# Performance work log

Measured on AMD Instinct MI355X. Metric: run time of the kernel, lower is better.

Reference implementation:

```python
import jax, jax.numpy as jnp
import numpy as np
import math

B, N, D, S = 128, 2048, 512, 64  # batch, nodes, d_model, state_features


def setup_inputs() -> dict:
    key = jax.random.key(0)
    k1, k2, k3, k4, k5 = jax.random.split(key, 5)
    node_embeddings = jax.random.normal(k1, (B, N, D), dtype=jnp.float32)
    truck_state = jax.random.normal(k2, (B, S), dtype=jnp.float32)
    mask = jax.random.bernoulli(k3, 0.3, (B, N))  # True = masked-out node
    Wq = jax.random.normal(k4, (D, S), dtype=jnp.float32) * 0.05  # query_proj weight
    bq = jnp.zeros((D,), dtype=jnp.float32)
    Ws = jax.random.normal(k5, (D, D), dtype=jnp.float32) * 0.02  # scores_proj weight
    bs = jnp.zeros((D,), dtype=jnp.float32)
    return {"node_embeddings": node_embeddings, "truck_state": truck_state,
            "mask": mask, "Wq": Wq, "bq": bq, "Ws": Ws, "bs": bs}


def reference(node_embeddings, truck_state, mask, Wq, bq, Ws, bs):
    d_model = node_embeddings.shape[-1]
    scale = 1.0 / math.sqrt(d_model)
    # query = query_proj(truck_state): [B, D]
    query = truck_state @ Wq.T + bq
    # single-query attention scores over nodes: [B, N]
    attn_scores = jnp.einsum('bd,bnd->bn', query, node_embeddings) * scale
    attn_scores = jnp.where(mask, -jnp.inf, attn_scores)
    attn_weights = jax.nn.softmax(attn_scores, axis=-1)
    # context: [B, D]
    context = jnp.einsum('bn,bnd->bd', attn_weights, node_embeddings)
    # scores = scores_proj(context): [B, D]
    scores = context @ Ws.T + bs
    # dot-product logits per node: [B, N]
    logits = jnp.einsum('bnd,bd->bn', node_embeddings, scores) * scale
    logits = jnp.where(mask, -jnp.inf, logits)
    return logits
```

## Files before the change

kernel.cpp:

```cpp
#include <hip/hip_runtime.h>
#include <math.h>

#define BB 128
#define NN 2048
#define DD 512
#define SS 64
#define NCH 16
#define CH (NN / NCH)
#define NPW (CH / 8)
#define SCALE 0.044194173824159216f
#define NEG_BIG (-1.0e30f)

__device__ __forceinline__ float dot8(float4 a0, float4 a1, float4 b0, float4 b1) {
    return a0.x*b0.x + a0.y*b0.y + a0.z*b0.z + a0.w*b0.w
         + a1.x*b1.x + a1.y*b1.y + a1.z*b1.z + a1.w*b1.w;
}

__global__ __launch_bounds__(512, 8) void k_pass1(
    const float* __restrict__ node, const unsigned char* __restrict__ mask,
    const float* __restrict__ ts, const float* __restrict__ Wq,
    const float* __restrict__ bq,
    float* __restrict__ part_ctx, float* __restrict__ part_l)
{
    int bid   = blockIdx.x;
    int b     = bid >> 4;
    int chunk = bid & 15;
    int wave  = threadIdx.x >> 6;
    int lane  = threadIdx.x & 63;
    int dbase = lane * 8;

    __shared__ float q_lds[DD];
    __shared__ float lds_ctx[8][DD];
    __shared__ float lds_l[8];

    {
        int d = threadIdx.x;
        const float4* tv = (const float4*)(ts + b * SS);
        const float4* wv = (const float4*)(Wq + (size_t)d * SS);
        float acc = 0.f;
#pragma unroll
        for (int k = 0; k < SS / 4; ++k) {
            float4 a = tv[k], w = wv[k];
            acc += a.x*w.x + a.y*w.y + a.z*w.z + a.w*w.w;
        }
        q_lds[d] = acc + bq[d];
    }

    int n0 = chunk * CH + wave * NPW;
    const unsigned char* mrow = mask + (size_t)b * NN;
    unsigned long long bal = __ballot(mrow[n0 + (lane & 15)] == 0);
    unsigned int lv = (unsigned int)(bal & 0xffffull);
    __syncthreads();

    float4 q0 = *(const float4*)&q_lds[dbase];
    float4 q1 = *(const float4*)&q_lds[dbase + 4];

    float l = 0.f;
    float c0=0,c1=0,c2=0,c3=0,c4=0,c5=0,c6=0,c7=0;
    const float* basep = node + ((size_t)b * NN + n0) * DD + dbase;

    while (lv) {
        int j0 = __ffs(lv) - 1; lv &= lv - 1;
        bool has2 = (lv != 0);
        int j1 = has2 ? (__ffs(lv) - 1) : j0;
        lv = has2 ? (lv & (lv - 1)) : lv;
        const float* r0 = basep + (size_t)j0 * DD;
        const float* r1 = basep + (size_t)j1 * DD;
        float4 v0a = *(const float4*)r0, v0b = *(const float4*)(r0 + 4);
        float4 v1a = *(const float4*)r1, v1b = *(const float4*)(r1 + 4);
        float dp0 = dot8(q0, q1, v0a, v0b);
        float dp1 = dot8(q0, q1, v1a, v1b);
#pragma unroll
        for (int off = 32; off; off >>= 1) {
            dp0 += __shfl_xor(dp0, off, 64);
            dp1 += __shfl_xor(dp1, off, 64);
        }
        float p0 = __expf(dp0 * SCALE);
        float p1 = has2 ? __expf(dp1 * SCALE) : 0.f;
        l += p0 + p1;
        c0 += p0*v0a.x + p1*v1a.x;
        c1 += p0*v0a.y + p1*v1a.y;
        c2 += p0*v0a.z + p1*v1a.z;
        c3 += p0*v0a.w + p1*v1a.w;
        c4 += p0*v0b.x + p1*v1b.x;
        c5 += p0*v0b.y + p1*v1b.y;
        c6 += p0*v0b.z + p1*v1b.z;
        c7 += p0*v0b.w + p1*v1b.w;
    }

    if (lane == 0) lds_l[wave] = l;
    *(float4*)&lds_ctx[wave][dbase]     = make_float4(c0, c1, c2, c3);
    *(float4*)&lds_ctx[wave][dbase + 4] = make_float4(c4, c5, c6, c7);
    __syncthreads();
    {
        int d = threadIdx.x;
        float acc = 0.f;
#pragma unroll
        for (int w = 0; w < 8; ++w) acc += lds_ctx[w][d];
        part_ctx[(size_t)bid * DD + d] = acc;
    }
    if (threadIdx.x == 0) {
        float L = 0.f;
#pragma unroll
        for (int w = 0; w < 8; ++w) L += lds_l[w];
        part_l[bid] = L;
    }
}

__global__ __launch_bounds__(256) void k_scores(
    const float* __restrict__ part_ctx, const float* __restrict__ part_l,
    const float* __restrict__ Ws, const float* __restrict__ bs,
    float* __restrict__ scores)
{
    int b    = blockIdx.x >> 2;
    int qt   = blockIdx.x & 3;
    int wave = threadIdx.x >> 6;
    int lane = threadIdx.x & 63;
    int dbase = lane * 8;
    __shared__ float ctx[DD];

    float L = 0.f;
#pragma unroll
    for (int c = 0; c < NCH; ++c) L += part_l[(b << 4) | c];
    float Linv = 1.f / fmaxf(L, 1e-30f);

    for (int d = threadIdx.x; d < DD; d += 256) {
        float acc = 0.f;
#pragma unroll
        for (int c = 0; c < NCH; ++c)
            acc += part_ctx[(size_t)((b << 4) | c) * DD + d];
        ctx[d] = acc * Linv;
    }
    __syncthreads();

    float4 x0 = *(const float4*)&ctx[dbase];
    float4 x1 = *(const float4*)&ctx[dbase + 4];
    for (int j = 0; j < 32; ++j) {
        int dd = qt * 128 + wave * 32 + j;
        const float* wrow = Ws + (size_t)dd * DD + dbase;
        float4 w0 = *(const float4*)wrow;
        float4 w1 = *(const float4*)(wrow + 4);
        float dp = dot8(x0, x1, w0, w1);
#pragma unroll
        for (int off = 32; off; off >>= 1) dp += __shfl_xor(dp, off, 64);
        if (lane == 0) scores[b * DD + dd] = dp + bs[dd];
    }
}

__global__ __launch_bounds__(256, 8) void k_logits(
    const float* __restrict__ node, const unsigned char* __restrict__ mask,
    const float* __restrict__ scores, float* __restrict__ out)
{
    int wave = threadIdx.x >> 6;
    int lane = threadIdx.x & 63;
    int dbase = lane * 8;
    int wg = blockIdx.x * 4 + wave;
    int rg = 32767 - wg;
    int g0 = rg * 8;
    int b  = g0 >> 11;

    unsigned long long mb = *(const unsigned long long*)(mask + g0);

    if (lane < 8 && ((mb >> (8 * lane)) & 0xffull)) out[g0 + lane] = NEG_BIG;

    unsigned int lv = 0;
#pragma unroll
    for (int i = 0; i < 8; ++i)
        lv |= (((mb >> (8 * i)) & 0xffull) == 0ull ? 1u : 0u) << i;

    const float* sc = scores + b * DD + dbase;
    float4 t0 = *(const float4*)sc;
    float4 t1 = *(const float4*)(sc + 4);
    const float* basep = node + (size_t)g0 * DD + dbase;

    while (lv) {
        int j0 = __ffs(lv) - 1; lv &= lv - 1;
        bool has2 = (lv != 0);
        int j1 = has2 ? (__ffs(lv) - 1) : j0;
        lv = has2 ? (lv & (lv - 1)) : lv;
        const float* r0 = basep + (size_t)j0 * DD;
        const float* r1 = basep + (size_t)j1 * DD;
        float4 v0a = *(const float4*)r0, v0b = *(const float4*)(r0 + 4);
        float4 v1a = *(const float4*)r1, v1b = *(const float4*)(r1 + 4);
        float dp0 = dot8(t0, t1, v0a, v0b);
        float dp1 = dot8(t0, t1, v1a, v1b);
#pragma unroll
        for (int off = 32; off; off >>= 1) {
            dp0 += __shfl_xor(dp0, off, 64);
            dp1 += __shfl_xor(dp1, off, 64);
        }
        if (lane == 0) {
            out[g0 + j0] = dp0 * SCALE;
            if (has2) out[g0 + j1] = dp1 * SCALE;
        }
    }
}

extern "C" void kernel_launch(void* const* d_in, const int* in_sizes, int n_in,
                              void* d_out, int out_size, void* d_ws, size_t ws_size,
                              hipStream_t stream)
{
    const float*         node = (const float*)d_in[0];
    const float*         ts   = (const float*)d_in[1];
    const unsigned char* mask = (const unsigned char*)d_in[2];
    const float*         Wq   = (const float*)d_in[3];
    const float*         bq   = (const float*)d_in[4];
    const float*         Ws   = (const float*)d_in[5];
    const float*         bs   = (const float*)d_in[6];
    float* out = (float*)d_out;

    float* ws       = (float*)d_ws;
    float* part_ctx = ws;
    float* part_l   = part_ctx + BB * NCH * DD;
    float* scores   = part_l + BB * NCH;

    k_pass1 <<<BB * NCH, 512, 0, stream>>>(node, mask, ts, Wq, bq,
                                           part_ctx, part_l);
    k_scores<<<BB * 4, 256, 0, stream>>>(part_ctx, part_l, Ws, bs, scores);
    k_logits<<<(BB * NN) / 32, 256, 0, stream>>>(node, mask, scores, out);
}
```

Before: 202.3 us.

## Balance unmasked rows across waves via block-level compacted node lists

Both node-streaming kernels now build a compacted list of unmasked node indices per block in shared memory using ballots and prefix popcounts. The rows are dealt round-robin across the waves, so each wave handles an even share instead of a fixed contiguous slice whose unmasked count varies. The intent is to cut wave-level load imbalance, where a block waits on its slowest wave. The cost is an extra barrier, shared-memory traffic for the list, and shuffles to fetch the row indices.

```diff
diff --git a/kernel.cpp b/kernel.cpp
--- a/kernel.cpp
+++ b/kernel.cpp
@@ -7,7 +7,6 @@
 #define SS 64
 #define NCH 16
 #define CH (NN / NCH)
-#define NPW (CH / 8)
 #define SCALE 0.044194173824159216f
 #define NEG_BIG (-1.0e30f)
 
@@ -28,10 +27,13 @@
     int wave  = threadIdx.x >> 6;
     int lane  = threadIdx.x & 63;
     int dbase = lane * 8;
+    int n0    = chunk * CH;
 
     __shared__ float q_lds[DD];
     __shared__ float lds_ctx[8][DD];
     __shared__ float lds_l[8];
+    __shared__ unsigned long long bal_lds[2];
+    __shared__ unsigned char list_lds[CH];
 
     {
         int d = threadIdx.x;
@@ -46,26 +48,47 @@
         q_lds[d] = acc + bq[d];
     }
 
-    int n0 = chunk * CH + wave * NPW;
-    const unsigned char* mrow = mask + (size_t)b * NN;
-    unsigned long long bal = __ballot(mrow[n0 + (lane & 15)] == 0);
-    unsigned int lv = (unsigned int)(bal & 0xffffull);
+    int t = threadIdx.x;
+    if (t < CH) {
+        bool ok = (mask[(size_t)b * NN + n0 + t] == 0);
+        unsigned long long balw = __ballot(ok);
+        if ((t & 63) == 0) bal_lds[t >> 6] = balw;
+    }
+    __syncthreads();
+    unsigned long long b0 = bal_lds[0], b1 = bal_lds[1];
+    int cnt0 = __popcll(b0);
+    int K    = cnt0 + __popcll(b1);
+    if (t < CH) {
+        bool ok = ((t < 64 ? b0 : b1) >> (t & 63)) & 1ull;
+        if (ok) {
+            int rank = (t < 64)
+                ? __popcll(b0 & ((1ull << t) - 1ull))
+                : cnt0 + __popcll(b1 & ((1ull << (t - 64)) - 1ull));
+            list_lds[rank] = (unsigned char)t;
+        }
+    }
     __syncthreads();
 
     float4 q0 = *(const float4*)&q_lds[dbase];
     float4 q1 = *(const float4*)&q_lds[dbase + 4];
+
+    int nmine = (K > wave) ? (K - wave + 7) >> 3 : 0;
+    int src = wave + 8 * (lane < 16 ? lane : 15);
+    if (src >= K) src = (K > 0) ? K - 1 : 0;
+    int myidx = list_lds[src];
 
     float l = 0.f;
     float c0=0,c1=0,c2=0,c3=0,c4=0,c5=0,c6=0,c7=0;
     const float* basep = node + ((size_t)b * NN + n0) * DD + dbase;
 
-    while (lv) {
-        int j0 = __ffs(lv) - 1; lv &= lv - 1;
-        bool has2 = (lv != 0);
-        int j1 = has2 ? (__ffs(lv) - 1) : j0;
-        lv = has2 ? (lv & (lv - 1)) : lv;
-        const float* r0 = basep + (size_t)j0 * DD;
-        const float* r1 = basep + (size_t)j1 * DD;
+    int npairs = (nmine + 1) >> 1;
+    for (int jp = 0; jp < npairs; ++jp) {
+        int j0 = 2 * jp, j1 = 2 * jp + 1;
+        bool has2 = (j1 < nmine);
+        int i0 = __shfl(myidx, j0);
+        int i1 = __shfl(myidx, has2 ? j1 : j0);
+        const float* r0 = basep + (size_t)i0 * DD;
+        const float* r1 = basep + (size_t)i1 * DD;
         float4 v0a = *(const float4*)r0, v0b = *(const float4*)(r0 + 4);
         float4 v1a = *(const float4*)r1, v1b = *(const float4*)(r1 + 4);
         float dp0 = dot8(q0, q1, v0a, v0b);
@@ -154,32 +177,51 @@
     int wave = threadIdx.x >> 6;
     int lane = threadIdx.x & 63;
     int dbase = lane * 8;
-    int wg = blockIdx.x * 4 + wave;
-    int rg = 32767 - wg;
-    int g0 = rg * 8;
-    int b  = g0 >> 11;
-
-    unsigned long long mb = *(const unsigned long long*)(mask + g0);
-
-    if (lane < 8 && ((mb >> (8 * lane)) & 0xffull)) out[g0 + lane] = NEG_BIG;
-
-    unsigned int lv = 0;
-#pragma unroll
-    for (int i = 0; i < 8; ++i)
-        lv |= (((mb >> (8 * i)) & 0xffull) == 0ull ? 1u : 0u) << i;
+    int blk  = 8191 - blockIdx.x;
+    int g0   = blk * 32;
+    int b    = g0 >> 11;
+
+    __shared__ unsigned int bal32;
+    __shared__ unsigned char list_lds[32];
+
+    int t = threadIdx.x;
+    bool okt = false;
+    if (t < 32) okt = (mask[g0 + t] == 0);
+    if (t < 64) {
+        unsigned long long bal = __ballot(okt);
+        if (t == 0) bal32 = (unsigned int)(bal & 0xffffffffull);
+    }
+    __syncthreads();
+    unsigned int lv = bal32;
+    int K = __popc(lv);
+
+    if (t < 32) {
+        if (!okt) out[g0 + t] = NEG_BIG;
+        else {
+            int rank = __popc(lv & ((1u << t) - 1u));
+            list_lds[rank] = (unsigned char)t;
+        }
+    }
+    __syncthreads();
+
+    int nmine = (K > wave) ? (K - wave + 3) >> 2 : 0;
+    int src = wave + 4 * (lane < 8 ? lane : 7);
+    if (src >= K) src = (K > 0) ? K - 1 : 0;
+    int myidx = list_lds[src];
 
     const float* sc = scores + b * DD + dbase;
     float4 t0 = *(const float4*)sc;
     float4 t1 = *(const float4*)(sc + 4);
     const float* basep = node + (size_t)g0 * DD + dbase;
 
-    while (lv) {
-        int j0 = __ffs(lv) - 1; lv &= lv - 1;
-        bool has2 = (lv != 0);
-        int j1 = has2 ? (__ffs(lv) - 1) : j0;
-        lv = has2 ? (lv & (lv - 1)) : lv;
-        const float* r0 = basep + (size_t)j0 * DD;
-        const float* r1 = basep + (size_t)j1 * DD;
+    int npairs = (nmine + 1) >> 1;
+    for (int jp = 0; jp < npairs; ++jp) {
+        int j0 = 2 * jp, j1 = 2 * jp + 1;
+        bool has2 = (j1 < nmine);
+        int i0 = __shfl(myidx, j0);
+        int i1 = __shfl(myidx, has2 ? j1 : j0);
+        const float* r0 = basep + (size_t)i0 * DD;
+        const float* r1 = basep + (size_t)i1 * DD;
         float4 v0a = *(const float4*)r0, v0b = *(const float4*)(r0 + 4);
         float4 v1a = *(const float4*)r1, v1b = *(const float4*)(r1 + 4);
         float dp0 = dot8(t0, t1, v0a, v0b);
@@ -190,8 +232,8 @@
             dp1 += __shfl_xor(dp1, off, 64);
         }
         if (lane == 0) {
-            out[g0 + j0] = dp0 * SCALE;
-            if (has2) out[g0 + j1] = dp1 * SCALE;
+            out[g0 + i0] = dp0 * SCALE;
+            if (has2) out[g0 + i1] = dp1 * SCALE;
         }
     }
 }
```

New measurement: 205.9 us. Within noise of the previous version (+1.8%).

## Fuse attention, scores projection and logits into one cooperative grid-synced kernel

Applied to the files above, without the earlier changes.

Moves the query projection into a separate small kernel and merges the pass-1 softmax/context accumulation, scores projection and logits pass into one cooperative kernel separated by grid-wide syncs. Each wave now handles 32 nodes and revisits the same rows in reverse order for the logits. This aims to remove launch gaps between stages and keep per-batch work local. It requires all 2048 blocks to be co-resident and adds grid barrier costs, with a three-kernel fallback if the cooperative launch fails.

```diff
diff --git a/kernel.cpp b/kernel.cpp
--- a/kernel.cpp
+++ b/kernel.cpp
@@ -1,13 +1,17 @@
 #include <hip/hip_runtime.h>
+#include <hip/hip_cooperative_groups.h>
 #include <math.h>
+
+namespace cg = cooperative_groups;
 
 #define BB 128
 #define NN 2048
 #define DD 512
 #define SS 64
-#define NCH 16
-#define CH (NN / NCH)
-#define NPW (CH / 8)
+#define NCHK 16
+#define CH 128
+#define NPW 32
+#define NBLK (BB * NCHK)
 #define SCALE 0.044194173824159216f
 #define NEG_BIG (-1.0e30f)
 
@@ -16,12 +20,31 @@
          + a1.x*b1.x + a1.y*b1.y + a1.z*b1.z + a1.w*b1.w;
 }
 
-__global__ __launch_bounds__(512, 8) void k_pass1(
+__global__ __launch_bounds__(512) void k_query(
+    const float* __restrict__ ts, const float* __restrict__ Wq,
+    const float* __restrict__ bq, float* __restrict__ query)
+{
+    int b = blockIdx.x;
+    int d = threadIdx.x;
+    const float4* tv = (const float4*)(ts + b * SS);
+    const float4* wv = (const float4*)(Wq + (size_t)d * SS);
+    float acc = 0.f;
+#pragma unroll
+    for (int k = 0; k < SS / 4; ++k) {
+        float4 a = tv[k], w = wv[k];
+        acc += a.x*w.x + a.y*w.y + a.z*w.z + a.w*w.w;
+    }
+    query[b * DD + d] = acc + bq[d];
+}
+
+__global__ __launch_bounds__(256, 8) void k_fused(
     const float* __restrict__ node, const unsigned char* __restrict__ mask,
-    const float* __restrict__ ts, const float* __restrict__ Wq,
-    const float* __restrict__ bq,
-    float* __restrict__ part_ctx, float* __restrict__ part_l)
-{
+    const float* __restrict__ query, const float* __restrict__ Ws,
+    const float* __restrict__ bs,
+    float* __restrict__ part_ctx, float* __restrict__ part_l,
+    float* __restrict__ scores, float* __restrict__ out)
+{
+    cg::grid_group grid = cg::this_grid();
     int bid   = blockIdx.x;
     int b     = bid >> 4;
     int chunk = bid & 15;
@@ -29,31 +52,17 @@
     int lane  = threadIdx.x & 63;
     int dbase = lane * 8;
 
-    __shared__ float q_lds[DD];
-    __shared__ float lds_ctx[8][DD];
-    __shared__ float lds_l[8];
-
-    {
-        int d = threadIdx.x;
-        const float4* tv = (const float4*)(ts + b * SS);
-        const float4* wv = (const float4*)(Wq + (size_t)d * SS);
-        float acc = 0.f;
-#pragma unroll
-        for (int k = 0; k < SS / 4; ++k) {
-            float4 a = tv[k], w = wv[k];
-            acc += a.x*w.x + a.y*w.y + a.z*w.z + a.w*w.w;
-        }
-        q_lds[d] = acc + bq[d];
-    }
+    __shared__ float lds_ctx[4][DD];
+    __shared__ float ctx_lds[DD];
+    __shared__ float lds_l[4];
+
+    float4 q0 = *(const float4*)(query + b * DD + dbase);
+    float4 q1 = *(const float4*)(query + b * DD + dbase + 4);
 
     int n0 = chunk * CH + wave * NPW;
-    const unsigned char* mrow = mask + (size_t)b * NN;
-    unsigned long long bal = __ballot(mrow[n0 + (lane & 15)] == 0);
-    unsigned int lv = (unsigned int)(bal & 0xffffull);
-    __syncthreads();
-
-    float4 q0 = *(const float4*)&q_lds[dbase];
-    float4 q1 = *(const float4*)&q_lds[dbase + 4];
+    unsigned long long bal = __ballot(mask[(size_t)b * NN + n0 + (lane & 31)] == 0);
+    unsigned int live = (unsigned int)(bal & 0xffffffffull);
+    unsigned int lv = live;
 
     float l = 0.f;
     float c0=0,c1=0,c2=0,c3=0,c4=0,c5=0,c6=0,c7=0;
@@ -78,16 +87,134 @@
         float p0 = __expf(dp0 * SCALE);
         float p1 = has2 ? __expf(dp1 * SCALE) : 0.f;
         l += p0 + p1;
-        c0 += p0*v0a.x + p1*v1a.x;
-        c1 += p0*v0a.y + p1*v1a.y;
-        c2 += p0*v0a.z + p1*v1a.z;
-        c3 += p0*v0a.w + p1*v1a.w;
-        c4 += p0*v0b.x + p1*v1b.x;
-        c5 += p0*v0b.y + p1*v1b.y;
-        c6 += p0*v0b.z + p1*v1b.z;
-        c7 += p0*v0b.w + p1*v1b.w;
-    }
-
+        c0 += p0*v0a.x + p1*v1a.x;  c1 += p0*v0a.y + p1*v1a.y;
+        c2 += p0*v0a.z + p1*v1a.z;  c3 += p0*v0a.w + p1*v1a.w;
+        c4 += p0*v0b.x + p1*v1b.x;  c5 += p0*v0b.y + p1*v1b.y;
+        c6 += p0*v0b.z + p1*v1b.z;  c7 += p0*v0b.w + p1*v1b.w;
+    }
+
+    if (lane == 0) lds_l[wave] = l;
+    *(float4*)&lds_ctx[wave][dbase]     = make_float4(c0, c1, c2, c3);
+    *(float4*)&lds_ctx[wave][dbase + 4] = make_float4(c4, c5, c6, c7);
+    __syncthreads();
+    for (int d = threadIdx.x; d < DD; d += 256) {
+        part_ctx[(size_t)bid * DD + d] =
+            lds_ctx[0][d] + lds_ctx[1][d] + lds_ctx[2][d] + lds_ctx[3][d];
+    }
+    if (threadIdx.x == 0)
+        part_l[bid] = lds_l[0] + lds_l[1] + lds_l[2] + lds_l[3];
+
+    grid.sync();
+
+    {
+        float L = 0.f;
+#pragma unroll
+        for (int c = 0; c < NCHK; ++c) L += part_l[(b << 4) | c];
+        float Linv = 1.f / fmaxf(L, 1e-30f);
+
+        for (int d = threadIdx.x; d < DD; d += 256) {
+            float acc = 0.f;
+#pragma unroll
+            for (int c = 0; c < NCHK; ++c)
+                acc += part_ctx[(size_t)((b << 4) | c) * DD + d];
+            ctx_lds[d] = acc * Linv;
+        }
+        __syncthreads();
+
+        float4 x0 = *(const float4*)&ctx_lds[dbase];
+        float4 x1 = *(const float4*)&ctx_lds[dbase + 4];
+        for (int j = 0; j < 8; ++j) {
+            int dd = chunk * 32 + wave * 8 + j;
+            const float* wrow = Ws + (size_t)dd * DD + dbase;
+            float4 w0 = *(const float4*)wrow;
+            float4 w1 = *(const float4*)(wrow + 4);
+            float dp = dot8(x0, x1, w0, w1);
+#pragma unroll
+            for (int off = 32; off; off >>= 1) dp += __shfl_xor(dp, off, 64);
+            if (lane == 0) scores[b * DD + dd] = dp + bs[dd];
+        }
+    }
+
+    grid.sync();
+
+    {
+        const float* sc = scores + b * DD + dbase;
+        float4 t0 = *(const float4*)sc;
+        float4 t1 = *(const float4*)(sc + 4);
+        int gb = b * NN + n0;
+
+        if (lane < 32 && !((live >> lane) & 1u)) out[gb + lane] = NEG_BIG;
+
+        unsigned int rv = live;
+        while (rv) {
+            int j0 = 31 - __clz(rv); rv &= ~(1u << j0);
+            bool has2 = (rv != 0);
+            int j1 = has2 ? (31 - __clz(rv)) : j0;
+            if (has2) rv &= ~(1u << j1);
+            const float* r0 = basep + (size_t)j0 * DD;
+            const float* r1 = basep + (size_t)j1 * DD;
+            float4 v0a = *(const float4*)r0, v0b = *(const float4*)(r0 + 4);
+            float4 v1a = *(const float4*)r1, v1b = *(const float4*)(r1 + 4);
+            float dp0 = dot8(t0, t1, v0a, v0b);
+            float dp1 = dot8(t0, t1, v1a, v1b);
+#pragma unroll
+            for (int off = 32; off; off >>= 1) {
+                dp0 += __shfl_xor(dp0, off, 64);
+                dp1 += __shfl_xor(dp1, off, 64);
+            }
+            if (lane == 0) {
+                out[gb + j0] = dp0 * SCALE;
+                if (has2) out[gb + j1] = dp1 * SCALE;
+            }
+        }
+    }
+}
+
+__global__ __launch_bounds__(512, 8) void k_pass1_fb(
+    const float* __restrict__ node, const unsigned char* __restrict__ mask,
+    const float* __restrict__ query,
+    float* __restrict__ part_ctx, float* __restrict__ part_l)
+{
+    int bid   = blockIdx.x;
+    int b     = bid >> 4;
+    int chunk = bid & 15;
+    int wave  = threadIdx.x >> 6;
+    int lane  = threadIdx.x & 63;
+    int dbase = lane * 8;
+    __shared__ float lds_ctx[8][DD];
+    __shared__ float lds_l[8];
+
+    float4 q0 = *(const float4*)(query + b * DD + dbase);
+    float4 q1 = *(const float4*)(query + b * DD + dbase + 4);
+    int n0 = chunk * CH + wave * (CH / 8);
+    unsigned long long bal = __ballot(mask[(size_t)b * NN + n0 + (lane & 15)] == 0);
+    unsigned int lv = (unsigned int)(bal & 0xffffull);
+    float l = 0.f, c0=0,c1=0,c2=0,c3=0,c4=0,c5=0,c6=0,c7=0;
+    const float* basep = node + ((size_t)b * NN + n0) * DD + dbase;
+    while (lv) {
+        int j0 = __ffs(lv) - 1; lv &= lv - 1;
+        bool has2 = (lv != 0);
+        int j1 = has2 ? (__ffs(lv) - 1) : j0;
+        lv = has2 ? (lv & (lv - 1)) : lv;
+        const float* r0 = basep + (size_t)j0 * DD;
+        const float* r1 = basep + (size_t)j1 * DD;
+        float4 v0a = *(const float4*)r0, v0b = *(const float4*)(r0 + 4);
+        float4 v1a = *(const float4*)r1, v1b = *(const float4*)(r1 + 4);
+        float dp0 = dot8(q0, q1, v0a, v0b);
+        float dp1 = dot8(q0, q1, v1a, v1b);
+#pragma unroll
+        for (int off = 32; off; off >>= 1) {
+            dp0 += __shfl_xor(dp0, off, 64);
+            dp1 += __shfl_xor(dp1, off, 64);
+        }
+        float p0 = __expf(dp0 * SCALE);
+        float p1 = has2 ? __expf(dp1 * SCALE) : 0.f;
+        l += p0 + p1;
+        c0 += p0*v0a.x + p1*v1a.x;  c1 += p0*v0a.y + p1*v1a.y;
+        c2 += p0*v0a.z + p1*v1a.z;  c3 += p0*v0a.w + p1*v1a.w;
+        c4 += p0*v0b.x + p1*v1b.x;  c5 += p0*v0b.y + p1*v1b.y;
+        c6 += p0*v0b.z + p1*v1b.z;  c7 += p0*v0b.w + p1*v1b.w;
+    }
     if (lane == 0) lds_l[wave] = l;
     *(float4*)&lds_ctx[wave][dbase]     = make_float4(c0, c1, c2, c3);
     *(float4*)&lds_ctx[wave][dbase + 4] = make_float4(c4, c5, c6, c7);
@@ -107,7 +234,7 @@
     }
 }
 
-__global__ __launch_bounds__(256) void k_scores(
+__global__ __launch_bounds__(256) void k_scores_fb(
     const float* __restrict__ part_ctx, const float* __restrict__ part_l,
     const float* __restrict__ Ws, const float* __restrict__ bs,
     float* __restrict__ scores)
@@ -118,21 +245,18 @@
     int lane = threadIdx.x & 63;
     int dbase = lane * 8;
     __shared__ float ctx[DD];
-
     float L = 0.f;
 #pragma unroll
-    for (int c = 0; c < NCH; ++c) L += part_l[(b << 4) | c];
+    for (int c = 0; c < NCHK; ++c) L += part_l[(b << 4) | c];
     float Linv = 1.f / fmaxf(L, 1e-30f);
-
     for (int d = threadIdx.x; d < DD; d += 256) {
         float acc = 0.f;
 #pragma unroll
-        for (int c = 0; c < NCH; ++c)
+        for (int c = 0; c < NCHK; ++c)
             acc += part_ctx[(size_t)((b << 4) | c) * DD + d];
         ctx[d] = acc * Linv;
     }
     __syncthreads();
-
     float4 x0 = *(const float4*)&ctx[dbase];
     float4 x1 = *(const float4*)&ctx[dbase + 4];
     for (int j = 0; j < 32; ++j) {
@@ -147,7 +271,7 @@
     }
 }
 
-__global__ __launch_bounds__(256, 8) void k_logits(
+__global__ __launch_bounds__(256, 8) void k_logits_fb(
     const float* __restrict__ node, const unsigned char* __restrict__ mask,
     const float* __restrict__ scores, float* __restrict__ out)
 {
@@ -158,21 +282,16 @@
     int rg = 32767 - wg;
     int g0 = rg * 8;
     int b  = g0 >> 11;
-
     unsigned long long mb = *(const unsigned long long*)(mask + g0);
-
     if (lane < 8 && ((mb >> (8 * lane)) & 0xffull)) out[g0 + lane] = NEG_BIG;
-
     unsigned int lv = 0;
 #pragma unroll
     for (int i = 0; i < 8; ++i)
         lv |= (((mb >> (8 * i)) & 0xffull) == 0ull ? 1u : 0u) << i;
-
     const float* sc = scores + b * DD + dbase;
     float4 t0 = *(const float4*)sc;
     float4 t1 = *(const float4*)(sc + 4);
     const float* basep = node + (size_t)g0 * DD + dbase;
-
     while (lv) {
         int j0 = __ffs(lv) - 1; lv &= lv - 1;
         bool has2 = (lv != 0);
@@ -211,11 +330,21 @@
 
     float* ws       = (float*)d_ws;
     float* part_ctx = ws;
-    float* part_l   = part_ctx + BB * NCH * DD;
-    float* scores   = part_l + BB * NCH;
-
-    k_pass1 <<<BB * NCH, 512, 0, stream>>>(node, mask, ts, Wq, bq,
-                                           part_ctx, part_l);
-    k_scores<<<BB * 4, 256, 0, stream>>>(part_ctx, part_l, Ws, bs, scores);
-    k_logits<<<(BB * NN) / 32, 256, 0, stream>>>(node, mask, scores, out);
-}
+    float* part_l   = part_ctx + (size_t)NBLK * DD;
+    float* scores   = part_l + NBLK;
+    float* query    = scores + BB * DD;
+
+    k_query<<<BB, 512, 0, stream>>>(ts, Wq, bq, query);
+
+    void* args[] = { (void*)&node, (void*)&mask, (void*)&query, (void*)&Ws,
+                     (void*)&bs, (void*)&part_ctx, (void*)&part_l,
+                     (void*)&scores, (void*)&out };
+    hipError_t err = hipLaunchCooperativeKernel((void*)k_fused, dim3(NBLK),
+                                                dim3(256), args, 0, stream);
+    if (err != hipSuccess) {
+        k_pass1_fb <<<NBLK, 512, 0, stream>>>(node, mask, query,
+                                              part_ctx, part_l);
+        k_scores_fb<<<BB * 4, 256, 0, stream>>>(part_ctx, part_l, Ws, bs, scores);
+        k_logits_fb<<<(BB * NN) / 32, 256, 0, stream>>>(node, mask, scores, out);
+    }
+}
```

Result: slower. 682.7 us (+237.4%).
